# Kernel tuning notes

Measured on AMD Instinct MI355X. Metric: run time of the kernel, lower is better.

Reference implementation:

```python
import jax, jax.numpy as jnp
import numpy as np

D_MODEL = 1024
NUM_HEADS = 16
D_K = D_MODEL // NUM_HEADS  # 64
THETA = 10000.0


def setup_inputs() -> dict:
    key = jax.random.key(0)
    k_x, k_q, k_k, k_v, k_o = jax.random.split(key, 5)
    B, S = 2, 2048
    std = (2.0 / (D_MODEL + D_MODEL)) ** 0.5
    x = jax.random.normal(k_x, (B, S, D_MODEL), dtype=jnp.float32)
    Wq = std * jax.random.truncated_normal(k_q, -3.0, 3.0, (D_MODEL, D_MODEL), dtype=jnp.float32)
    Wk = std * jax.random.truncated_normal(k_k, -3.0, 3.0, (D_MODEL, D_MODEL), dtype=jnp.float32)
    Wv = std * jax.random.truncated_normal(k_v, -3.0, 3.0, (D_MODEL, D_MODEL), dtype=jnp.float32)
    Wo = std * jax.random.truncated_normal(k_o, -3.0, 3.0, (D_MODEL, D_MODEL), dtype=jnp.float32)
    return {"x": x, "Wq": Wq, "Wk": Wk, "Wv": Wv, "Wo": Wo}


def _apply_rope(t, cos, sin):
    # t: [B, H, S, d_k]; cos/sin: [S, d_k//2] broadcast over B, H
    tr = t.reshape(*t.shape[:-1], D_K // 2, 2)
    t1, t2 = tr[..., 0], tr[..., 1]
    r1 = t1 * cos - t2 * sin
    r2 = t1 * sin + t2 * cos
    return jnp.stack([r1, r2], axis=-1).reshape(t.shape)


def reference(x, Wq, Wk, Wv, Wo):
    B, S, D = x.shape
    H, dk = NUM_HEADS, D_K
    # projections (no bias): y = x @ W.T
    Q = (x @ Wq.T).reshape(B, S, H, dk).transpose(0, 2, 1, 3)  # [B,H,S,dk]
    K = (x @ Wk.T).reshape(B, S, H, dk).transpose(0, 2, 1, 3)
    V = (x @ Wv.T).reshape(B, S, H, dk).transpose(0, 2, 1, 3)
    # RoPE angles for positions 0..S-1
    pos = jnp.arange(S, dtype=jnp.float32)[:, None]            # [S,1]
    freqs = 1.0 / (THETA ** (jnp.arange(0, dk, 2, dtype=jnp.float32) / dk))  # [dk/2]
    angles = pos * freqs[None, :]                              # [S, dk/2]
    cos, sin = jnp.cos(angles), jnp.sin(angles)
    Q = _apply_rope(Q, cos, sin)
    K = _apply_rope(K, cos, sin)
    # causal scaled dot-product attention
    scores = jnp.einsum("bhqd,bhkd->bhqk", Q, K) / jnp.sqrt(jnp.float32(dk))
    causal = jnp.tril(jnp.ones((S, S), dtype=bool))
    scores = jnp.where(causal, scores, -jnp.inf)
    probs = jax.nn.softmax(scores, axis=-1)
    attn = jnp.einsum("bhqk,bhkd->bhqd", probs, V)             # [B,H,S,dk]
    attn = attn.transpose(0, 2, 1, 3).reshape(B, S, H * dk)
    return attn @ Wo.T
```

## Files before the change

kernel.cpp:

```cpp
#include <hip/hip_runtime.h>
#include <hip/hip_bf16.h>

typedef __bf16 bf16;
typedef __bf16 bf16x8 __attribute__((ext_vector_type(8)));
typedef float f32x4 __attribute__((ext_vector_type(4)));

#define MFMA16(A, B, C) __builtin_amdgcn_mfma_f32_16x16x32_bf16((A), (B), (C), 0, 0, 0)

static __device__ __forceinline__ void gload16(const bf16* g, bf16* l) {
    __builtin_amdgcn_global_load_lds((const __attribute__((address_space(1))) void*)g,
                                     (__attribute__((address_space(3))) void*)l, 16, 0, 0);
}

__global__ void detect_kernel(const void* w, int* flag) {
    float v = (float)((const bf16*)w)[threadIdx.x];
    unsigned long long bad = __ballot(!(fabsf(v) < 1.0f));
    if (threadIdx.x == 0) *flag = bad ? 1 : 0;
}

__global__ __launch_bounds__(256) void convert_all(const void* x, const void* w0,
                                                   const void* w1, const void* w2,
                                                   const void* w3, bf16* xb, bf16* b0,
                                                   bf16* b1, bf16* b2, bf16* b3,
                                                   const int* flagp) {
    if (*flagp == 0) return;
    int id = (blockIdx.x * 256 + threadIdx.x) * 4;
    const int XN = 1 << 22;
    const float* src;
    bf16* dst;
    int off;
    if (id < XN) {
        src = (const float*)x; dst = xb; off = id;
    } else {
        int r = id - XN;
        int wi = r >> 20;
        off = r & ((1 << 20) - 1);
        src = (const float*)(wi == 0 ? w0 : wi == 1 ? w1 : wi == 2 ? w2 : w3);
        dst = (wi == 0 ? b0 : wi == 1 ? b1 : wi == 2 ? b2 : b3);
    }
    float4 v = *(const float4*)(src + off);
    bf16 o[4] = {(bf16)v.x, (bf16)v.y, (bf16)v.z, (bf16)v.w};
    *(uint2*)(dst + off) = *(uint2*)o;
}

__global__ __launch_bounds__(512, 2) void qkv_gemm(const void* rawA, const bf16* convA,
                                                   const void* rW0, const bf16* cW0,
                                                   const void* rW1, const bf16* cW1,
                                                   const void* rW2, const bf16* cW2,
                                                   bf16* Qo, bf16* Ko, bf16* Vt,
                                                   const int* flagp) {
    const int K = 1024;
    const int NS = 32;
    __shared__ __attribute__((aligned(16))) bf16 lsA[3][256 * 32];
    __shared__ __attribute__((aligned(16))) bf16 lsB[3][256 * 32];
    const int flag = *flagp;
    const bf16* A = flag ? convA : (const bf16*)rawA;

    const int swz = (blockIdx.x & 7) * 24 + (blockIdx.x >> 3);
    const int m0 = (swz / 12) * 256;
    const int bxn = swz % 12;
    const int tensor = bxn >> 2;
    const int n0 = (bxn & 3) * 256;
    const bf16* W = tensor == 0 ? (flag ? cW0 : (const bf16*)rW0)
                  : tensor == 1 ? (flag ? cW1 : (const bf16*)rW1)
                                : (flag ? cW2 : (const bf16*)rW2);

    const int t = threadIdx.x;
    const int w = t >> 6, lane = t & 63;
    const int wr = w >> 2, wc = w & 3;
    const int llo = lane & 15, quad = lane >> 4;
    const int sel = (llo >> 1) & 3;

    f32x4 acc[8][4] = {};

    auto stage = [&](int s, int slot) {
#pragma unroll
        for (int j = 0; j < 2; ++j) {
            int c = j * 512 + t;
            int row = c >> 2, pos = c & 3;
            int g = pos ^ ((row >> 1) & 3);
            gload16(A + (size_t)(m0 + row) * K + s * 32 + g * 8, &lsA[slot][c * 8]);
        }
#pragma unroll
        for (int j = 0; j < 2; ++j) {
            int c = j * 512 + t;
            int row = c >> 2, pos = c & 3;
            int g = pos ^ ((row >> 1) & 3);
            gload16(W + (size_t)(n0 + row) * K + s * 32 + g * 8, &lsB[slot][c * 8]);
        }
    };

    stage(0, 0);
    stage(1, 1);
    asm volatile("s_waitcnt vmcnt(4)" ::: "memory");
    __builtin_amdgcn_s_barrier();
    __builtin_amdgcn_sched_barrier(0);

    int cur = 0;
    for (int it = 0; it < NS; ++it) {
        bf16x8 a[8], bb[4];
#pragma unroll
        for (int mi = 0; mi < 8; ++mi) {
            int r = wr * 128 + mi * 16 + llo;
            a[mi] = *(const bf16x8*)&lsA[cur][r * 32 + ((quad ^ sel) * 8)];
        }
#pragma unroll
        for (int ni = 0; ni < 4; ++ni) {
            int r = wc * 64 + ni * 16 + llo;
            bb[ni] = *(const bf16x8*)&lsB[cur][r * 32 + ((quad ^ sel) * 8)];
        }
        if (it + 2 < NS) {
            int ns = cur + 2;
            if (ns >= 3) ns -= 3;
            stage(it + 2, ns);
        }
#pragma unroll
        for (int mi = 0; mi < 8; ++mi)
#pragma unroll
            for (int ni = 0; ni < 4; ++ni)
                acc[mi][ni] = MFMA16(a[mi], bb[ni], acc[mi][ni]);
        if (it < NS - 2) {
            asm volatile("s_waitcnt vmcnt(4)" ::: "memory");
        } else {
            asm volatile("s_waitcnt vmcnt(0)" ::: "memory");
        }
        __builtin_amdgcn_s_barrier();
        __builtin_amdgcn_sched_barrier(0);
        cur = cur + 1;
        if (cur >= 3) cur = 0;
    }

#pragma unroll
    for (int mi = 0; mi < 8; ++mi)
#pragma unroll
        for (int ni = 0; ni < 4; ++ni)
#pragma unroll
            for (int r = 0; r < 4; ++r) {
                int row = m0 + wr * 128 + mi * 16 + quad * 4 + r;
                int col = n0 + wc * 64 + ni * 16 + llo;
                float v = acc[mi][ni][r];
                if (tensor == 2) {
                    int b = row >> 11, srow = row & 2047;
                    Vt[((size_t)b * 1024 + col) * 2048 + srow] = (bf16)v;
                } else {
                    int d = col & 63, srow = row & 2047;
                    float partner = __shfl_xor(v, 1);
                    float freq = exp2f((float)(d >> 1) * -0.4152410118609203f);
                    float rev = (float)srow * freq * 0.15915494309189535f;
                    rev -= floorf(rev);
                    float sn = __builtin_amdgcn_sinf(rev);
                    float cs = __builtin_amdgcn_cosf(rev);
                    float outv = v * cs + partner * sn * ((d & 1) ? 1.0f : -1.0f);
                    bf16* dst = (tensor == 0) ? Qo : Ko;
                    dst[(size_t)row * 1024 + col] = (bf16)outv;
                }
            }
}

template <int MODE>
__global__ __launch_bounds__(256, 3) void gemm_nt(const void* rawA, const bf16* convA,
                                                  const void* rW0, const bf16* cW0,
                                                  const void* rW1, const bf16* cW1,
                                                  const void* rW2, const bf16* cW2,
                                                  bf16* Qo, bf16* Ko, bf16* Vt,
                                                  float* p0, float* p1,
                                                  const int* flagp) {
    const int K = 1024;
    __shared__ __attribute__((aligned(16))) bf16 lsA[2][128 * 32];
    __shared__ __attribute__((aligned(16))) bf16 lsB[2][128 * 32];
    const int flag = *flagp;
    const bf16* A = flag ? convA : (const bf16*)rawA;
    int tensor, n0, m0, ks;
    const bf16* W;
    if (MODE == 0) {
        tensor = blockIdx.x >> 3;
        n0 = (blockIdx.x & 7) * 128;
        m0 = blockIdx.y * 128;
        ks = 0;
        W = tensor == 0 ? (flag ? cW0 : (const bf16*)rW0)
          : tensor == 1 ? (flag ? cW1 : (const bf16*)rW1)
                        : (flag ? cW2 : (const bf16*)rW2);
    } else {
        const int bid = blockIdx.x;
        ks = bid & 1;
        const int slot = bid >> 1;
        m0 = (slot & 31) * 128;
        n0 = (slot >> 5) * 128;
        tensor = 0;
        W = flag ? cW0 : (const bf16*)rW0;
    }
    const int t = threadIdx.x;
    const int w = t >> 6, lane = t & 63;
    const int wr = w >> 1, wc = w & 1;
    const int llo = lane & 15, quad = lane >> 4;
    const int sel = (llo >> 1) & 3;

    f32x4 acc[4][4] = {};

    auto stage = [&](int k0, int buf) {
#pragma unroll
        for (int j = 0; j < 2; ++j) {
            int c = j * 256 + t;
            int row = c >> 2, pos = c & 3;
            int g = pos ^ ((row >> 1) & 3);
            gload16(A + (size_t)(m0 + row) * K + k0 + g * 8, &lsA[buf][c * 8]);
        }
#pragma unroll
        for (int j = 0; j < 2; ++j) {
            int c = j * 256 + t;
            int row = c >> 2, pos = c & 3;
            int g = pos ^ ((row >> 1) & 3);
            gload16(W + (size_t)(n0 + row) * K + k0 + g * 8, &lsB[buf][c * 8]);
        }
    };

    auto compute = [&](int buf) {
        bf16x8 a[4], bb[4];
#pragma unroll
        for (int mi = 0; mi < 4; ++mi) {
            int r = wr * 64 + mi * 16 + llo;
            a[mi] = *(const bf16x8*)&lsA[buf][r * 32 + ((quad ^ sel) * 8)];
        }
#pragma unroll
        for (int ni = 0; ni < 4; ++ni) {
            int r = wc * 64 + ni * 16 + llo;
            bb[ni] = *(const bf16x8*)&lsB[buf][r * 32 + ((quad ^ sel) * 8)];
        }
#pragma unroll
        for (int mi = 0; mi < 4; ++mi)
#pragma unroll
            for (int ni = 0; ni < 4; ++ni)
                acc[mi][ni] = MFMA16(a[mi], bb[ni], acc[mi][ni]);
    };

    const int kbase = (MODE == 1) ? ks * 512 : 0;
    const int NIT = (MODE == 1) ? 16 : 32;

    stage(kbase, 0);
    for (int it = 0; it < NIT; it += 2) {
        __syncthreads();
        stage(kbase + (it + 1) * 32, 1);
        compute(0);
        __syncthreads();
        if (it + 2 < NIT) stage(kbase + (it + 2) * 32, 0);
        compute(1);
    }

#pragma unroll
    for (int mi = 0; mi < 4; ++mi)
#pragma unroll
        for (int ni = 0; ni < 4; ++ni)
#pragma unroll
            for (int r = 0; r < 4; ++r) {
                int row = m0 + wr * 64 + mi * 16 + quad * 4 + r;
                int col = n0 + wc * 64 + ni * 16 + llo;
                float v = acc[mi][ni][r];
                if (MODE == 1) {
                    float* dst = ks ? p1 : p0;
                    dst[(size_t)row * 1024 + col] = v;
                } else if (tensor == 2) {
                    int b = row >> 11, s = row & 2047;
                    Vt[((size_t)b * 1024 + col) * 2048 + s] = (bf16)v;
                } else {
                    int d = col & 63, s = row & 2047;
                    float partner = __shfl_xor(v, 1);
                    float freq = exp2f((float)(d >> 1) * -0.4152410118609203f);
                    float rev = (float)s * freq * 0.15915494309189535f;
                    rev -= floorf(rev);
                    float sn = __builtin_amdgcn_sinf(rev);
                    float cs = __builtin_amdgcn_cosf(rev);
                    float outv = v * cs + partner * sn * ((d & 1) ? 1.0f : -1.0f);
                    bf16* dst = (tensor == 0) ? Qo : Ko;
                    dst[(size_t)row * 1024 + col] = (bf16)outv;
                }
            }
}

__global__ __launch_bounds__(256) void reduce_out(const float* p0, const float* p1,
                                                  void* dout, const int* flagp) {
    int i = (blockIdx.x * 256 + threadIdx.x) * 4;
    float4 a = *(const float4*)(p0 + i);
    float4 b = *(const float4*)(p1 + i);
    float4 s = {a.x + b.x, a.y + b.y, a.z + b.z, a.w + b.w};
    if (*flagp) {
        *(float4*)((float*)dout + i) = s;
    } else {
        bf16 o[4] = {(bf16)s.x, (bf16)s.y, (bf16)s.z, (bf16)s.w};
        *(uint2*)((bf16*)dout + i) = *(uint2*)o;
    }
}

__global__ __launch_bounds__(256, 3) void attn_kernel(const bf16* __restrict__ Q,
                                                      const bf16* __restrict__ Kr,
                                                      const bf16* __restrict__ Vt,
                                                      bf16* __restrict__ O,
                                                      bf16* __restrict__ Opart,
                                                      float* __restrict__ lws) {
    __shared__ __attribute__((aligned(16))) bf16 lsK[2][64 * 64];
    __shared__ __attribute__((aligned(16))) bf16 lsV[2][64 * 64];
    __shared__ __attribute__((aligned(16))) bf16 lsP[4][32 * 64];
    const int blk = blockIdx.x;
    int ib, bh, s, tt0, tt1;
    bool split;
    if (blk < 512) {
        split = true;
        s = blk >> 8;
        int c = blk & 255;
        ib = 15 - (c >> 5);
        bh = c & 31;
        tt0 = s ? (ib + 1) : 0;
        tt1 = s ? (2 * ib + 1) : ib;
    } else {
        split = false;
        s = 0;
        int c = blk - 512;
        ib = c >> 5;
        bh = c & 31;
        tt0 = 0;
        tt1 = 2 * ib + 1;
    }
    const int b = bh >> 4, h = bh & 15;
    const int t = threadIdx.x, w = t >> 6, lane = t & 63;
    const int llo = lane & 15, quad = lane >> 4;
    const int q0w = ib * 128 + w * 32;

    bf16x8 aQ[2][2];
#pragma unroll
    for (int qi = 0; qi < 2; ++qi) {
        const size_t qb =
            ((size_t)(b * 2048 + q0w + qi * 16 + llo)) * 1024 + h * 64 + quad * 8;
        aQ[qi][0] = *(const bf16x8*)&Q[qb];
        aQ[qi][1] = *(const bf16x8*)&Q[qb + 32];
    }

    f32x4 o[2][4] = {};
    float lpart[2] = {0.f, 0.f};
    const float SC = 0.18033688011112042f;
    const int qlane0 = q0w + llo;

    const int srow8 = lane >> 3;
    const int sc = (lane & 7) ^ srow8;

    auto stage = [&](int tt, int buf) {
        const int kv0 = tt * 64;
#pragma unroll
        for (int jj = 0; jj < 2; ++jj) {
            int seg = w + jj * 4;
            int rowk = seg * 8 + srow8;
            gload16(&Kr[((size_t)(b * 2048 + kv0 + rowk)) * 1024 + h * 64 + sc * 8],
                    &lsK[buf][seg * 512 + lane * 8]);
            gload16(&Vt[((size_t)(b * 1024 + h * 64 + rowk)) * 2048 + kv0 + sc * 8],
                    &lsV[buf][seg * 512 + lane * 8]);
        }
    };

    stage(tt0, 0);

    for (int tt = tt0; tt <= tt1; ++tt) {
        const int cur = (tt - tt0) & 1;
        const int kv0 = tt * 64;
        __syncthreads();
        if (tt + 1 <= tt1) stage(tt + 1, cur ^ 1);

        if (kv0 <= q0w + 31) {
            bf16x8 kf[4][2];
#pragma unroll
            for (int half = 0; half < 4; ++half) {
                int rk = half * 16 + llo;
                kf[half][0] = *(const bf16x8*)&lsK[cur][rk * 64 + ((quad ^ (rk & 7)) * 8)];
                kf[half][1] =
                    *(const bf16x8*)&lsK[cur][rk * 64 + (((quad + 4) ^ (rk & 7)) * 8)];
            }
            bf16x8 vf[2][4];
#pragma unroll
            for (int kc = 0; kc < 2; ++kc)
#pragma unroll
                for (int g = 0; g < 4; ++g) {
                    int rv = g * 16 + llo;
                    int cg = kc * 4 + quad;
                    vf[kc][g] =
                        *(const bf16x8*)&lsV[cur][rv * 64 + ((cg ^ (rv & 7)) * 8)];
                }

            const bool need_mask = (kv0 + 63 >= q0w);
#pragma unroll
            for (int qi = 0; qi < 2; ++qi) {
                const int q = qlane0 + qi * 16;
                const int prow = qi * 16 + llo;
#pragma unroll
                for (int half = 0; half < 4; ++half) {
                    f32x4 z = {};
                    z = MFMA16(kf[half][0], aQ[qi][0], z);
                    z = MFMA16(kf[half][1], aQ[qi][1], z);
                    union { bf16 hh[4]; uint2 uu; } pk;
                    if (need_mask) {
                        int kvb = kv0 + half * 16 + quad * 4;
#pragma unroll
                        for (int r = 0; r < 4; ++r) {
                            float e = (kvb + r <= q) ? z[r] * SC : -INFINITY;
                            float p = __builtin_amdgcn_exp2f(e);
                            lpart[qi] += p;
                            pk.hh[r] = (bf16)p;
                        }
                    } else {
#pragma unroll
                        for (int r = 0; r < 4; ++r) {
                            float p = __builtin_amdgcn_exp2f(z[r] * SC);
                            lpart[qi] += p;
                            pk.hh[r] = (bf16)p;
                        }
                    }
                    int cw = 2 * half + (quad >> 1);
                    *(uint2*)&lsP[w][prow * 64 + ((cw ^ (llo & 7)) * 8) + (quad & 1) * 4] =
                        pk.uu;
                }
            }
            __builtin_amdgcn_wave_barrier();
#pragma unroll
            for (int qi = 0; qi < 2; ++qi) {
                const int prow = qi * 16 + llo;
#pragma unroll
                for (int kc = 0; kc < 2; ++kc) {
                    int cr = 4 * kc + quad;
                    bf16x8 aP =
                        *(const bf16x8*)&lsP[w][prow * 64 + ((cr ^ (llo & 7)) * 8)];
#pragma unroll
                    for (int g = 0; g < 4; ++g) o[qi][g] = MFMA16(aP, vf[kc][g], o[qi][g]);
                }
            }
            __builtin_amdgcn_wave_barrier();
        }
    }

    float lfull[2];
#pragma unroll
    for (int qi = 0; qi < 2; ++qi) {
        float l = lpart[qi];
        l += __shfl_xor(l, 16);
        l += __shfl_xor(l, 32);
        lfull[qi] = l;
    }

    if (split) {
        const int slotw = ((ib - 8) * 32 + bh) * 2 + s;
        bf16* op = Opart + (size_t)slotw * 8192;
#pragma unroll
        for (int qi = 0; qi < 2; ++qi) {
#pragma unroll
            for (int r = 0; r < 4; ++r) {
                int row_in = w * 32 + qi * 16 + quad * 4 + r;
#pragma unroll
                for (int g = 0; g < 4; ++g)
                    op[row_in * 64 + g * 16 + llo] = (bf16)o[qi][g][r];
            }
            if (quad == 0) lws[slotw * 128 + w * 32 + qi * 16 + llo] = lfull[qi];
        }
    } else {
#pragma unroll
        for (int qi = 0; qi < 2; ++qi)
#pragma unroll
            for (int r = 0; r < 4; ++r) {
                float l = __shfl(lfull[qi], (lane & 48) | (quad * 4 + r));
                float inv = 1.f / l;
                int q = q0w + qi * 16 + quad * 4 + r;
                size_t ob = ((size_t)(b * 2048 + q)) * 1024 + h * 64;
#pragma unroll
                for (int g = 0; g < 4; ++g)
                    O[ob + g * 16 + llo] = (bf16)(o[qi][g][r] * inv);
            }
    }
}

__global__ __launch_bounds__(256) void combine_kernel(const bf16* __restrict__ Opart,
                                                      const float* __restrict__ lws,
                                                      bf16* __restrict__ AO) {
    int id = blockIdx.x * 256 + threadIdx.x;
    int d = id & 63;
    int h = (id >> 6) & 15;
    int qoff = (id >> 10) & 1023;
    int b = id >> 20;
    int ib8 = qoff >> 7;
    int q_in = qoff & 127;
    int slot = (ib8 * 32 + (b * 16 + h)) * 2;
    size_t base = (size_t)slot * 8192 + q_in * 64 + d;
    float o0 = (float)Opart[base];
    float o1 = (float)Opart[base + 8192];
    float l = lws[slot * 128 + q_in] + lws[(slot + 1) * 128 + q_in];
    int q = 1024 + qoff;
    AO[((size_t)(b * 2048 + q)) * 1024 + h * 64 + d] = (bf16)((o0 + o1) / l);
}

extern "C" void kernel_launch(void* const* d_in, const int* in_sizes, int n_in,
                              void* d_out, int out_size, void* d_ws, size_t ws_size,
                              hipStream_t stream) {
    const size_t TN = (size_t)4096 * 1024;

    int* flag = (int*)d_ws;
    bf16* Q = (bf16*)((char*)d_ws + 256);
    bf16* Kb = Q + TN;
    bf16* Vt = Kb + TN;
    bf16* xb = Vt + TN;
    bf16* Wb0 = xb + TN;
    bf16* Wb1 = Wb0 + TN / 4;
    bf16* Wb2 = Wb1 + TN / 4;
    bf16* Wb3 = Wb2 + TN / 4;
    bf16* AO = Q;
    bf16* Opart = xb;
    float* lws = (float*)Wb0;
    float* p0 = (float*)Kb;
    float* p1 = (float*)xb;

    detect_kernel<<<1, 64, 0, stream>>>(d_in[1], flag);
    convert_all<<<8192, 256, 0, stream>>>(d_in[0], d_in[1], d_in[2], d_in[3], d_in[4],
                                          xb, Wb0, Wb1, Wb2, Wb3, flag);

    qkv_gemm<<<192, 512, 0, stream>>>(d_in[0], xb, d_in[1], Wb0, d_in[2], Wb1,
                                      d_in[3], Wb2, Q, Kb, Vt, flag);

    attn_kernel<<<768, 256, 0, stream>>>(Q, Kb, Vt, AO, Opart, lws);
    combine_kernel<<<8192, 256, 0, stream>>>(Opart, lws, AO);

    gemm_nt<1><<<512, 256, 0, stream>>>(AO, AO, d_in[4], Wb3, nullptr, nullptr,
                                        nullptr, nullptr, nullptr, nullptr, nullptr,
                                        p0, p1, flag);
    reduce_out<<<4096, 256, 0, stream>>>(p0, p1, d_out, flag);
}
```

Baseline: 202.6 us.

## Split QKV GEMM main loop into two phases with staggered loads and setprio

The QKV projection GEMM loop is split into two half-tiles of MFMA work. The A-tile global-to-LDS prefetch is issued before the first half and the B-tile prefetch before the second, and s_setprio raises wave priority around each MFMA block. This interleaves memory issue with compute across waves, ping-pong style, to hide load latency and shrink register pressure from the A fragments. It adds extra barriers per iteration, which may cost synchronisation overhead.

```diff
diff --git a/kernel.cpp b/kernel.cpp
--- a/kernel.cpp
+++ b/kernel.cpp
@@ -73,7 +73,7 @@
 
     f32x4 acc[8][4] = {};
 
-    auto stage = [&](int s, int slot) {
+    auto stageA = [&](int s, int slot) {
 #pragma unroll
         for (int j = 0; j < 2; ++j) {
             int c = j * 512 + t;
@@ -81,6 +81,8 @@
             int g = pos ^ ((row >> 1) & 3);
             gload16(A + (size_t)(m0 + row) * K + s * 32 + g * 8, &lsA[slot][c * 8]);
         }
+    };
+    auto stageB = [&](int s, int slot) {
 #pragma unroll
         for (int j = 0; j < 2; ++j) {
             int c = j * 512 + t;
@@ -90,17 +92,19 @@
         }
     };
 
-    stage(0, 0);
-    stage(1, 1);
+    stageA(0, 0); stageB(0, 0);
+    stageA(1, 1); stageB(1, 1);
     asm volatile("s_waitcnt vmcnt(4)" ::: "memory");
     __builtin_amdgcn_s_barrier();
     __builtin_amdgcn_sched_barrier(0);
 
     int cur = 0;
     for (int it = 0; it < NS; ++it) {
-        bf16x8 a[8], bb[4];
-#pragma unroll
-        for (int mi = 0; mi < 8; ++mi) {
+        int ns = cur + 2;
+        if (ns >= 3) ns -= 3;
+        bf16x8 a[4], bb[4];
+#pragma unroll
+        for (int mi = 0; mi < 4; ++mi) {
             int r = wr * 128 + mi * 16 + llo;
             a[mi] = *(const bf16x8*)&lsA[cur][r * 32 + ((quad ^ sel) * 8)];
         }
@@ -109,21 +113,40 @@
             int r = wc * 64 + ni * 16 + llo;
             bb[ni] = *(const bf16x8*)&lsB[cur][r * 32 + ((quad ^ sel) * 8)];
         }
-        if (it + 2 < NS) {
-            int ns = cur + 2;
-            if (ns >= 3) ns -= 3;
-            stage(it + 2, ns);
-        }
-#pragma unroll
-        for (int mi = 0; mi < 8; ++mi)
+        if (it + 2 < NS) stageA(it + 2, ns);
+        __builtin_amdgcn_s_barrier();
+        __builtin_amdgcn_sched_barrier(0);
+        __builtin_amdgcn_s_setprio(1);
+#pragma unroll
+        for (int mi = 0; mi < 4; ++mi)
 #pragma unroll
             for (int ni = 0; ni < 4; ++ni)
                 acc[mi][ni] = MFMA16(a[mi], bb[ni], acc[mi][ni]);
+        __builtin_amdgcn_s_setprio(0);
+        __builtin_amdgcn_s_barrier();
+        __builtin_amdgcn_sched_barrier(0);
+
+        bf16x8 a2[4];
+#pragma unroll
+        for (int mi = 0; mi < 4; ++mi) {
+            int r = wr * 128 + (mi + 4) * 16 + llo;
+            a2[mi] = *(const bf16x8*)&lsA[cur][r * 32 + ((quad ^ sel) * 8)];
+        }
+        if (it + 2 < NS) stageB(it + 2, ns);
         if (it < NS - 2) {
             asm volatile("s_waitcnt vmcnt(4)" ::: "memory");
         } else {
             asm volatile("s_waitcnt vmcnt(0)" ::: "memory");
         }
+        __builtin_amdgcn_s_barrier();
+        __builtin_amdgcn_sched_barrier(0);
+        __builtin_amdgcn_s_setprio(1);
+#pragma unroll
+        for (int mi = 0; mi < 4; ++mi)
+#pragma unroll
+            for (int ni = 0; ni < 4; ++ni)
+                acc[mi + 4][ni] = MFMA16(a2[mi], bb[ni], acc[mi + 4][ni]);
+        __builtin_amdgcn_s_setprio(0);
         __builtin_amdgcn_s_barrier();
         __builtin_amdgcn_sched_barrier(0);
         cur = cur + 1;
```

After: 206.1 us. About the same (+1.7%).
